# Kernel tuning notes

Hardware: AMD Instinct MI355X
Metric: run time of the kernel (lower is better)

The kernel has to match this reference:

```python
import jax, jax.numpy as jnp
import numpy as np

B, T, D = 2, 2048, 1024
D_LABEL = D // 2
N_LABELS = 50


def setup_inputs() -> dict:
    key = jax.random.key(0)
    ks = jax.random.split(key, 10)
    dep = jax.random.normal(ks[0], (B, T, D), dtype=jnp.float32)
    head = jax.random.normal(ks[1], (B, T + 1, D), dtype=jnp.float32)
    head_indices = jax.random.randint(ks[2], (B, T), 0, T + 1)
    mask = jnp.ones((B, T), dtype=bool)
    # learned params
    lim_p = 1.0 / np.sqrt(D)
    dep_W = jax.random.uniform(ks[3], (D_LABEL, D), minval=-lim_p, maxval=lim_p, dtype=jnp.float32)
    dep_b = jax.random.uniform(ks[4], (D_LABEL,), minval=-lim_p, maxval=lim_p, dtype=jnp.float32)
    head_W = jax.random.uniform(ks[5], (D_LABEL, D), minval=-lim_p, maxval=lim_p, dtype=jnp.float32)
    head_b = jax.random.uniform(ks[6], (D_LABEL,), minval=-lim_p, maxval=lim_p, dtype=jnp.float32)
    # xavier_uniform over last two dims of W
    lim_w = np.sqrt(6.0 / (D_LABEL + D_LABEL))
    W = jax.random.uniform(ks[7], (N_LABELS, D_LABEL, D_LABEL), minval=-lim_w, maxval=lim_w, dtype=jnp.float32)
    bias = jnp.zeros((N_LABELS,), dtype=jnp.float32)
    return {"dep": dep, "head": head, "head_indices": head_indices, "mask": mask,
            "dep_W": dep_W, "dep_b": dep_b, "head_W": head_W, "head_b": head_b,
            "W": W, "bias": bias}


def reference(dep, head, head_indices, mask, dep_W, dep_b, head_W, head_b, W, bias):
    # project to label space [B,T,d_label] / [B,T+1,d_label]
    dep_label = jnp.einsum('btd,ed->bte', dep, dep_W) + dep_b
    head_label = jnp.einsum('btd,ed->bte', head, head_W) + head_b
    # gather predicted head rep per token: [B,T,d_label]
    selected = jnp.take_along_axis(head_label, head_indices[..., None], axis=1)
    # biaffine scoring: dep^T W_n head for each label n -> [B,T,n_labels]
    logits = jnp.einsum('btd,nde,bte->btn', dep_label, W, selected)
    return logits + bias[None, None, :]
```

## Files before the change

kernel.cpp:

```cpp
#include <hip/hip_runtime.h>
#include <hip/hip_bf16.h>
#include <cstdint>

typedef __bf16 bf16;
typedef bf16 bf16x8 __attribute__((ext_vector_type(8)));
typedef float f32x4 __attribute__((ext_vector_type(4)));

#define NTOK 4096
#define DLBL 512
#define NLAB 50

__device__ inline bf16x8 cvt8(float4 a, float4 b) {
  bf16x8 r;
  r[0] = (bf16)a.x; r[1] = (bf16)a.y; r[2] = (bf16)a.z; r[3] = (bf16)a.w;
  r[4] = (bf16)b.x; r[5] = (bf16)b.y; r[6] = (bf16)b.z; r[7] = (bf16)b.w;
  return r;
}

__device__ __forceinline__ void gl16(const bf16* g, void* l) {
  __builtin_amdgcn_global_load_lds(
      (const __attribute__((address_space(1))) void*)g,
      (__attribute__((address_space(3))) void*)l, 16, 0, 0);
}

__device__ void projA_body(int bidx, const float* __restrict__ Wp,
                           const float* __restrict__ X,
                           const float* __restrict__ bv,
                           bf16* __restrict__ outT, char* lds) {
  char* ldsA = lds;
  char* ldsB = lds + 10240;
  const int tid = threadIdx.x, l = tid & 63, w = tid >> 6;
  const int tokbase = (bidx >> 2) * 64;
  const int ebase   = (bidx & 3) * 128;
  const int wr = w & 1, wc = w >> 1;
  f32x4 acc[4][2] = {};
  const int arow = tid >> 1, ahalf = tid & 1;
  const int brow = tid >> 2, bgr = tid & 3;
  const float* aS = Wp + (size_t)(ebase + arow) * 1024 + ahalf * 16;
  const float* bS = X  + (size_t)(tokbase + brow) * 1024 + bgr * 8;
  const int lo = (l & 15) * 80 + (l >> 4) * 16;
  for (int kb = 0; kb < 1024; kb += 32) {
    float4 a0 = *(const float4*)(aS + kb);
    float4 a1 = *(const float4*)(aS + kb + 4);
    float4 a2 = *(const float4*)(aS + kb + 8);
    float4 a3 = *(const float4*)(aS + kb + 12);
    float4 b0 = *(const float4*)(bS + kb);
    float4 b1 = *(const float4*)(bS + kb + 4);
    *(bf16x8*)(ldsA + arow * 80 + ahalf * 32)      = cvt8(a0, a1);
    *(bf16x8*)(ldsA + arow * 80 + ahalf * 32 + 16) = cvt8(a2, a3);
    *(bf16x8*)(ldsB + brow * 80 + bgr * 16)        = cvt8(b0, b1);
    __syncthreads();
    bf16x8 aF[4], bF[2];
#pragma unroll
    for (int i = 0; i < 4; ++i) aF[i] = *(bf16x8*)(ldsA + (wr * 64 + i * 16) * 80 + lo);
#pragma unroll
    for (int j = 0; j < 2; ++j) bF[j] = *(bf16x8*)(ldsB + (wc * 32 + j * 16) * 80 + lo);
#pragma unroll
    for (int i = 0; i < 4; ++i)
#pragma unroll
      for (int j = 0; j < 2; ++j)
        acc[i][j] = __builtin_amdgcn_mfma_f32_16x16x32_bf16(aF[i], bF[j], acc[i][j], 0, 0, 0);
    __syncthreads();
  }
#pragma unroll
  for (int i = 0; i < 4; ++i)
#pragma unroll
    for (int j = 0; j < 2; ++j)
#pragma unroll
      for (int r = 0; r < 4; ++r) {
        int eg = ebase + wr * 64 + i * 16 + (l >> 4) * 4 + r;
        int tg = tokbase + wc * 32 + j * 16 + (l & 15);
        outT[(size_t)eg * NTOK + tg] = (bf16)(acc[i][j][r] + bv[eg]);
      }
}

__device__ void projB_body(int bidx, const float* __restrict__ head,
                           const int* __restrict__ hidx,
                           const float* __restrict__ Wp,
                           const float* __restrict__ bv,
                           bf16* __restrict__ selO, char* lds) {
  char* ldsA = lds;
  char* ldsB = lds + 10240;
  const int tid = threadIdx.x, l = tid & 63, w = tid >> 6;
  const int tokbase = (bidx >> 3) * 128;
  const int ebase   = (bidx & 7) * 64;
  const int wr = w & 1, wc = w >> 1;
  f32x4 acc[4][2] = {};
  const int arow = tid >> 1, ahalf = tid & 1;
  const int brow = tid >> 2, bgr = tid & 3;
  const int flat = tokbase + arow;
  const int bb = flat >> 11;
  const int hv = hidx[flat];
  const float* aS = head + ((size_t)bb * 2049 + hv) * 1024 + ahalf * 16;
  const float* bS = Wp + (size_t)(ebase + brow) * 1024 + bgr * 8;
  const int lo = (l & 15) * 80 + (l >> 4) * 16;
  for (int kb = 0; kb < 1024; kb += 32) {
    float4 a0 = *(const float4*)(aS + kb);
    float4 a1 = *(const float4*)(aS + kb + 4);
    float4 a2 = *(const float4*)(aS + kb + 8);
    float4 a3 = *(const float4*)(aS + kb + 12);
    float4 b0 = *(const float4*)(bS + kb);
    float4 b1 = *(const float4*)(bS + kb + 4);
    *(bf16x8*)(ldsA + arow * 80 + ahalf * 32)      = cvt8(a0, a1);
    *(bf16x8*)(ldsA + arow * 80 + ahalf * 32 + 16) = cvt8(a2, a3);
    *(bf16x8*)(ldsB + brow * 80 + bgr * 16)        = cvt8(b0, b1);
    __syncthreads();
    bf16x8 aF[4], bF[2];
#pragma unroll
    for (int i = 0; i < 4; ++i) aF[i] = *(bf16x8*)(ldsA + (wr * 64 + i * 16) * 80 + lo);
#pragma unroll
    for (int j = 0; j < 2; ++j) bF[j] = *(bf16x8*)(ldsB + (wc * 32 + j * 16) * 80 + lo);
#pragma unroll
    for (int i = 0; i < 4; ++i)
#pragma unroll
      for (int j = 0; j < 2; ++j)
        acc[i][j] = __builtin_amdgcn_mfma_f32_16x16x32_bf16(aF[i], bF[j], acc[i][j], 0, 0, 0);
    __syncthreads();
  }
#pragma unroll
  for (int i = 0; i < 4; ++i)
#pragma unroll
    for (int j = 0; j < 2; ++j)
#pragma unroll
      for (int r = 0; r < 4; ++r) {
        int tg = tokbase + wr * 64 + i * 16 + (l >> 4) * 4 + r;
        int eg = ebase + wc * 32 + j * 16 + (l & 15);
        selO[(size_t)tg * DLBL + eg] = (bf16)(acc[i][j][r] + bv[eg]);
      }
}

__global__ __launch_bounds__(256) void prep_k(const float* __restrict__ W,
                                              bf16* __restrict__ Wb,
                                              const float* __restrict__ dep_W,
                                              const float* __restrict__ dep,
                                              const float* __restrict__ dep_b,
                                              bf16* __restrict__ depT,
                                              const float* __restrict__ head,
                                              const int* __restrict__ hidx,
                                              const float* __restrict__ head_W,
                                              const float* __restrict__ head_b,
                                              bf16* __restrict__ selB) {
  __shared__ char lds[15360];
  const int b = blockIdx.x;
  if (b < 256) {
    projA_body(b, dep_W, dep, dep_b, depT, lds);
  } else if (b < 512) {
    projB_body(b - 256, head, hidx, head_W, head_b, selB, lds);
  } else {
    int i = (b - 512) * 256 + threadIdx.x;
    const float4* s = (const float4*)W + (size_t)i * 2;
    float4 a = s[0], c = s[1];
    *(bf16x8*)(Wb + (size_t)i * 8) = cvt8(a, c);
  }
}

__global__ __launch_bounds__(256, 2) void biaff_k(const bf16* __restrict__ Wb,
                                                  const bf16* __restrict__ sel,
                                                  const bf16* __restrict__ depT,
                                                  float* __restrict__ parts) {
  __shared__ char lds[73728];
  const int tid = threadIdx.x, l = tid & 63, w = tid >> 6;

  const int lin = blockIdx.x;
  const int xcd = lin & 7, idx = lin >> 3;
  const int sub = idx % 25;
  const int bx  = idx / 25;
  const int combo = xcd * 25 + sub;
  const int n  = combo % 50;
  const int dz = combo / 50;
  const int tokbase = bx * 256;
  const int dbase   = dz * 128;

  const int wd = w >> 1, wt = w & 1;
  f32x4 acc[4][8] = {};

  const int srow = l >> 2;
  const int schunk = ((l & 3) ^ ((l >> 3) & 3)) * 8;
  const bf16* aG = Wb  + ((size_t)(n * DLBL + dbase + w * 32 + srow)) * DLBL + schunk;
  const bf16* bG = sel + ((size_t)(tokbase + w * 64 + srow)) * DLBL + schunk;
  const int aOff = w * 2048;
  const int bOff = 8192 + w * 4096;

  const int lq = l & 15, lh = l >> 4;
  const int ro = lh ^ ((lq >> 1) & 3);
  const char* rdA = lds + (wd * 64 + lq) * 64 + ro * 16;
  const char* rdB = lds + 8192 + (wt * 128 + lq) * 64 + ro * 16;

#define STG(T) do { \
    const bf16* a_ = aG + (T) * 32; \
    const bf16* b_ = bG + (T) * 32; \
    char* la_ = lds + ((T) % 3) * 24576 + aOff; \
    char* lb_ = lds + ((T) % 3) * 24576 + bOff; \
    gl16(a_, la_);            gl16(a_ + 16 * DLBL, la_ + 1024); \
    gl16(b_, lb_);            gl16(b_ + 16 * DLBL, lb_ + 1024); \
    gl16(b_ + 32 * DLBL, lb_ + 2048); gl16(b_ + 48 * DLBL, lb_ + 3072); \
  } while (0)
#define WAITV(N) asm volatile("s_waitcnt vmcnt(" #N ")" ::: "memory")
#define PHASE(T, DOSTG, DOWV6, DOWV0, DOBAR) do { \
    const char* cA = rdA + ((T) % 3) * 24576; \
    const char* cB = rdB + ((T) % 3) * 24576; \
    bf16x8 aF[4], bF[8]; \
    _Pragma("unroll") \
    for (int i = 0; i < 4; ++i) aF[i] = *(const bf16x8*)(cA + i * 1024); \
    _Pragma("unroll") \
    for (int j = 0; j < 8; ++j) bF[j] = *(const bf16x8*)(cB + j * 1024); \
    if (DOSTG) STG((T) + 2); \
    __builtin_amdgcn_s_setprio(1); \
    _Pragma("unroll") \
    for (int i = 0; i < 4; ++i) \
      _Pragma("unroll") \
      for (int j = 0; j < 8; ++j) \
        acc[i][j] = __builtin_amdgcn_mfma_f32_16x16x32_bf16(aF[i], bF[j], acc[i][j], 0, 0, 0); \
    __builtin_amdgcn_s_setprio(0); \
    if (DOWV6) WAITV(6); \
    if (DOWV0) WAITV(0); \
    if (DOBAR) __builtin_amdgcn_s_barrier(); \
  } while (0)

  STG(0); STG(1);
  WAITV(6);
  __builtin_amdgcn_s_barrier();

  PHASE(0, 1, 1, 0, 1);  PHASE(1, 1, 1, 0, 1);  PHASE(2, 1, 1, 0, 1);
  PHASE(3, 1, 1, 0, 1);  PHASE(4, 1, 1, 0, 1);  PHASE(5, 1, 1, 0, 1);
  PHASE(6, 1, 1, 0, 1);  PHASE(7, 1, 1, 0, 1);  PHASE(8, 1, 1, 0, 1);
  PHASE(9, 1, 1, 0, 1);  PHASE(10, 1, 1, 0, 1); PHASE(11, 1, 1, 0, 1);
  PHASE(12, 1, 1, 0, 1); PHASE(13, 1, 1, 0, 1);
  PHASE(14, 0, 0, 1, 1);
  PHASE(15, 0, 0, 0, 0);

#undef PHASE
#undef WAITV
#undef STG

  float p[8] = {0.f, 0.f, 0.f, 0.f, 0.f, 0.f, 0.f, 0.f};
#pragma unroll
  for (int j = 0; j < 8; ++j) {
    const int tg = tokbase + wt * 128 + j * 16 + lq;
#pragma unroll
    for (int i = 0; i < 4; ++i)
#pragma unroll
      for (int r = 0; r < 4; ++r) {
        int dg = dbase + wd * 64 + i * 16 + lh * 4 + r;
        p[j] += acc[i][j][r] * (float)depT[(size_t)dg * NTOK + tg];
      }
  }
#pragma unroll
  for (int j = 0; j < 8; ++j) {
    p[j] += __shfl_xor(p[j], 16);
    p[j] += __shfl_xor(p[j], 32);
  }
  if (l < 16) {
#pragma unroll
    for (int j = 0; j < 8; ++j) {
      int tg = tokbase + wt * 128 + j * 16 + l;
      parts[(size_t)(dz * 2 + wd) * 204800 + (size_t)tg * NLAB + n] = p[j];
    }
  }
}

__global__ __launch_bounds__(256) void fin_k(const float* __restrict__ parts,
                                             const float* __restrict__ bias,
                                             float* __restrict__ out) {
  int i = blockIdx.x * 256 + threadIdx.x;
  float v = 0.f;
#pragma unroll
  for (int q = 0; q < 8; ++q) v += parts[(size_t)q * 204800 + i];
  out[i] = v + bias[i % NLAB];
}

extern "C" void kernel_launch(void* const* d_in, const int* in_sizes, int n_in,
                              void* d_out, int out_size, void* d_ws, size_t ws_size,
                              hipStream_t stream) {
  const float* dep    = (const float*)d_in[0];
  const float* head   = (const float*)d_in[1];
  const int*   hidx   = (const int*)d_in[2];
  const float* dep_W  = (const float*)d_in[4];
  const float* dep_b  = (const float*)d_in[5];
  const float* head_W = (const float*)d_in[6];
  const float* head_b = (const float*)d_in[7];
  const float* W      = (const float*)d_in[8];
  const float* bias   = (const float*)d_in[9];
  float* out = (float*)d_out;

  char* ws = (char*)d_ws;
  bf16*  Wb    = (bf16*)(ws);
  bf16*  depT  = (bf16*)(ws + 26214400);
  bf16*  selB  = (bf16*)(ws + 30408704);
  float* parts = (float*)(ws + 34603008);
  if (ws_size < (size_t)41156608) return;

  hipLaunchKernelGGL(prep_k, dim3(6912), dim3(256), 0, stream,
                     W, Wb, dep_W, dep, dep_b, depT, head, hidx, head_W, head_b, selB);
  hipLaunchKernelGGL(biaff_k, dim3(3200), dim3(256), 0, stream, Wb, selB, depT, parts);
  hipLaunchKernelGGL(fin_k, dim3(800), dim3(256), 0, stream, parts, bias, out);
}
```

Baseline: 163.3 us.

## Enlarge biaffine GEMM tile to 256x256 with 512-thread blocks and double buffering

The biaffine kernel now uses 512-thread blocks that each compute a 256(d) x 256(token) tile, replacing the 128x256 tile, with K steps of 64 split into two half-steps and a 2-stage LDS double buffer instead of a 3-stage ring. The grid is halved and the XCD-to-block mapping is reworked so paired XCDs share label slices across token blocks. Fewer d-splits mean fewer partial sums to write and to reduce in fin_k. In exchange, each block holds 128 KB of LDS and more barriers per K step, which could lower occupancy and expose more load latency.

New measurement: 177.3 us. +8.6%, slower.

```diff
diff --git a/kernel.cpp b/kernel.cpp
--- a/kernel.cpp
+++ b/kernel.cpp
@@ -154,107 +154,126 @@
   }
 }
 
-__global__ __launch_bounds__(256, 2) void biaff_k(const bf16* __restrict__ Wb,
+__global__ __launch_bounds__(512, 2) void biaff_k(const bf16* __restrict__ Wb,
                                                   const bf16* __restrict__ sel,
                                                   const bf16* __restrict__ depT,
                                                   float* __restrict__ parts) {
-  __shared__ char lds[73728];
+  __shared__ char lds[131072];
   const int tid = threadIdx.x, l = tid & 63, w = tid >> 6;
 
   const int lin = blockIdx.x;
-  const int xcd = lin & 7, idx = lin >> 3;
-  const int sub = idx % 25;
-  const int bx  = idx / 25;
-  const int combo = xcd * 25 + sub;
+  const int xcd = lin & 7, j5 = lin >> 3;
+  const int g = xcd >> 1, h = xcd & 1;
+  const int combo = g * 25 + (j5 % 25);
+  const int bx = (j5 / 25) * 2 + h;
   const int n  = combo % 50;
   const int dz = combo / 50;
   const int tokbase = bx * 256;
-  const int dbase   = dz * 128;
-
-  const int wd = w >> 1, wt = w & 1;
-  f32x4 acc[4][8] = {};
+
+  const int wd = w >> 2, wt = w & 3;
+  f32x4 acc[8][4] = {};
 
   const int srow = l >> 2;
   const int schunk = ((l & 3) ^ ((l >> 3) & 3)) * 8;
-  const bf16* aG = Wb  + ((size_t)(n * DLBL + dbase + w * 32 + srow)) * DLBL + schunk;
-  const bf16* bG = sel + ((size_t)(tokbase + w * 64 + srow)) * DLBL + schunk;
+  const bf16* aG = Wb  + ((size_t)(n * DLBL + dz * 256 + w * 32 + srow)) * DLBL + schunk;
+  const bf16* bG = sel + ((size_t)(tokbase + w * 32 + srow)) * DLBL + schunk;
   const int aOff = w * 2048;
-  const int bOff = 8192 + w * 4096;
 
   const int lq = l & 15, lh = l >> 4;
   const int ro = lh ^ ((lq >> 1) & 3);
-  const char* rdA = lds + (wd * 64 + lq) * 64 + ro * 16;
-  const char* rdB = lds + 8192 + (wt * 128 + lq) * 64 + ro * 16;
-
-#define STG(T) do { \
-    const bf16* a_ = aG + (T) * 32; \
-    const bf16* b_ = bG + (T) * 32; \
-    char* la_ = lds + ((T) % 3) * 24576 + aOff; \
-    char* lb_ = lds + ((T) % 3) * 24576 + bOff; \
-    gl16(a_, la_);            gl16(a_ + 16 * DLBL, la_ + 1024); \
-    gl16(b_, lb_);            gl16(b_ + 16 * DLBL, lb_ + 1024); \
-    gl16(b_ + 32 * DLBL, lb_ + 2048); gl16(b_ + 48 * DLBL, lb_ + 3072); \
+  const char* rdA = lds + (wd * 128 + lq) * 64 + ro * 16;
+  const char* rdB = lds + 16384 + (wt * 64 + lq) * 64 + ro * 16;
+
+#define STG_A(T, KK) do { \
+    const bf16* s_ = aG + (T) * 64 + (KK) * 32; \
+    char* d_ = lds + (((T) & 1) * 65536) + (KK) * 32768 + aOff; \
+    gl16(s_, d_); gl16(s_ + 16 * DLBL, d_ + 1024); \
+  } while (0)
+#define STG_B(T, KK) do { \
+    const bf16* s_ = bG + (T) * 64 + (KK) * 32; \
+    char* d_ = lds + (((T) & 1) * 65536) + 16384 + (KK) * 32768 + aOff; \
+    gl16(s_, d_); gl16(s_ + 16 * DLBL, d_ + 1024); \
   } while (0)
 #define WAITV(N) asm volatile("s_waitcnt vmcnt(" #N ")" ::: "memory")
-#define PHASE(T, DOSTG, DOWV6, DOWV0, DOBAR) do { \
-    const char* cA = rdA + ((T) % 3) * 24576; \
-    const char* cB = rdB + ((T) % 3) * 24576; \
-    bf16x8 aF[4], bF[8]; \
-    _Pragma("unroll") \
-    for (int i = 0; i < 4; ++i) aF[i] = *(const bf16x8*)(cA + i * 1024); \
-    _Pragma("unroll") \
-    for (int j = 0; j < 8; ++j) bF[j] = *(const bf16x8*)(cB + j * 1024); \
-    if (DOSTG) STG((T) + 2); \
+#define RDA(KK, M) do { _Pragma("unroll") for (int i = 0; i < 4; ++i) \
+    aF[i] = *(const bf16x8*)(rdA + cb + (KK) * 32768 + (M) * 4096 + i * 1024); } while (0)
+#define RDB(KK) do { _Pragma("unroll") for (int jj = 0; jj < 4; ++jj) \
+    bF[jj] = *(const bf16x8*)(rdB + cb + (KK) * 32768 + jj * 1024); } while (0)
+#define MM(M) do { \
     __builtin_amdgcn_s_setprio(1); \
-    _Pragma("unroll") \
-    for (int i = 0; i < 4; ++i) \
-      _Pragma("unroll") \
-      for (int j = 0; j < 8; ++j) \
-        acc[i][j] = __builtin_amdgcn_mfma_f32_16x16x32_bf16(aF[i], bF[j], acc[i][j], 0, 0, 0); \
+    _Pragma("unroll") for (int i = 0; i < 4; ++i) \
+      _Pragma("unroll") for (int jj = 0; jj < 4; ++jj) \
+        acc[(M) * 4 + i][jj] = __builtin_amdgcn_mfma_f32_16x16x32_bf16(aF[i], bF[jj], acc[(M) * 4 + i][jj], 0, 0, 0); \
     __builtin_amdgcn_s_setprio(0); \
-    if (DOWV6) WAITV(6); \
-    if (DOWV0) WAITV(0); \
-    if (DOBAR) __builtin_amdgcn_s_barrier(); \
   } while (0)
-
-  STG(0); STG(1);
-  WAITV(6);
-  __builtin_amdgcn_s_barrier();
-
-  PHASE(0, 1, 1, 0, 1);  PHASE(1, 1, 1, 0, 1);  PHASE(2, 1, 1, 0, 1);
-  PHASE(3, 1, 1, 0, 1);  PHASE(4, 1, 1, 0, 1);  PHASE(5, 1, 1, 0, 1);
-  PHASE(6, 1, 1, 0, 1);  PHASE(7, 1, 1, 0, 1);  PHASE(8, 1, 1, 0, 1);
-  PHASE(9, 1, 1, 0, 1);  PHASE(10, 1, 1, 0, 1); PHASE(11, 1, 1, 0, 1);
-  PHASE(12, 1, 1, 0, 1); PHASE(13, 1, 1, 0, 1);
-  PHASE(14, 0, 0, 1, 1);
-  PHASE(15, 0, 0, 0, 0);
-
-#undef PHASE
+#define BAR __builtin_amdgcn_s_barrier()
+
+#define TILE(T, DOSTG, V1, DOV3) do { \
+    const int cb = ((T) & 1) * 65536; \
+    bf16x8 aF[4], bF[4]; \
+     \
+    RDA(0, 0); RDB(0); \
+    if (DOSTG) STG_A((T) + 1, 0); \
+    BAR; MM(0); BAR; \
+     \
+    RDA(0, 1); \
+    if (DOSTG) STG_B((T) + 1, 0); \
+    BAR; MM(1); WAITV(V1); BAR; \
+     \
+    RDA(1, 0); RDB(1); \
+    if (DOSTG) STG_A((T) + 1, 1); \
+    BAR; MM(0); BAR; \
+     \
+    RDA(1, 1); \
+    if (DOSTG) STG_B((T) + 1, 1); \
+    BAR; MM(1); \
+    if (DOV3) { WAITV(4); } \
+    if (DOV3) { BAR; } \
+  } while (0)
+
+  STG_A(0, 0); STG_B(0, 0); STG_A(0, 1); STG_B(0, 1);
+  WAITV(0);
+  BAR;
+
+  TILE(0, 1, 4, 1);
+  TILE(1, 1, 4, 1);
+  TILE(2, 1, 4, 1);
+  TILE(3, 1, 4, 1);
+  TILE(4, 1, 4, 1);
+  TILE(5, 1, 4, 1);
+  TILE(6, 1, 4, 1);
+  TILE(7, 0, 0, 0);
+
+#undef TILE
+#undef BAR
+#undef MM
+#undef RDB
+#undef RDA
 #undef WAITV
-#undef STG
-
-  float p[8] = {0.f, 0.f, 0.f, 0.f, 0.f, 0.f, 0.f, 0.f};
-#pragma unroll
-  for (int j = 0; j < 8; ++j) {
-    const int tg = tokbase + wt * 128 + j * 16 + lq;
-#pragma unroll
-    for (int i = 0; i < 4; ++i)
-#pragma unroll
-      for (int r = 0; r < 4; ++r) {
-        int dg = dbase + wd * 64 + i * 16 + lh * 4 + r;
-        p[j] += acc[i][j][r] * (float)depT[(size_t)dg * NTOK + tg];
-      }
-  }
-#pragma unroll
-  for (int j = 0; j < 8; ++j) {
-    p[j] += __shfl_xor(p[j], 16);
-    p[j] += __shfl_xor(p[j], 32);
+#undef STG_B
+#undef STG_A
+
+  const bf16* dT = depT + (size_t)(dz * 256 + wd * 128) * NTOK;
+  float p[4] = {0.f, 0.f, 0.f, 0.f};
+#pragma unroll
+  for (int jj = 0; jj < 4; ++jj) {
+    const int tg = tokbase + wt * 64 + jj * 16 + lq;
+#pragma unroll
+    for (int i = 0; i < 8; ++i)
+#pragma unroll
+      for (int r = 0; r < 4; ++r)
+        p[jj] += acc[i][jj][r] * (float)dT[(size_t)(i * 16 + lh * 4 + r) * NTOK + tg];
+  }
+#pragma unroll
+  for (int jj = 0; jj < 4; ++jj) {
+    p[jj] += __shfl_xor(p[jj], 16);
+    p[jj] += __shfl_xor(p[jj], 32);
   }
   if (l < 16) {
 #pragma unroll
-    for (int j = 0; j < 8; ++j) {
-      int tg = tokbase + wt * 128 + j * 16 + l;
-      parts[(size_t)(dz * 2 + wd) * 204800 + (size_t)tg * NLAB + n] = p[j];
+    for (int jj = 0; jj < 4; ++jj) {
+      int tg = tokbase + wt * 64 + jj * 16 + l;
+      parts[(size_t)(dz * 2 + wd) * 204800 + (size_t)tg * NLAB + n] = p[jj];
     }
   }
 }
@@ -265,7 +284,7 @@
   int i = blockIdx.x * 256 + threadIdx.x;
   float v = 0.f;
 #pragma unroll
-  for (int q = 0; q < 8; ++q) v += parts[(size_t)q * 204800 + i];
+  for (int q = 0; q < 4; ++q) v += parts[(size_t)q * 204800 + i];
   out[i] = v + bias[i % NLAB];
 }
 
@@ -288,10 +307,10 @@
   bf16*  depT  = (bf16*)(ws + 26214400);
   bf16*  selB  = (bf16*)(ws + 30408704);
   float* parts = (float*)(ws + 34603008);
-  if (ws_size < (size_t)41156608) return;
+  if (ws_size < (size_t)37879808) return;
 
   hipLaunchKernelGGL(prep_k, dim3(6912), dim3(256), 0, stream,
                      W, Wb, dep_W, dep, dep_b, depT, head, hidx, head_W, head_b, selB);
-  hipLaunchKernelGGL(biaff_k, dim3(3200), dim3(256), 0, stream, Wb, selB, depT, parts);
+  hipLaunchKernelGGL(biaff_k, dim3(1600), dim3(512), 0, stream, Wb, selB, depT, parts);
   hipLaunchKernelGGL(fin_k, dim3(800), dim3(256), 0, stream, parts, bias, out);
 }
```

## Switch biaffine kernel to 32x32 MFMA with 8 waves and in-block reduction

Applied to the files above, without the earlier changes.

The biaffine kernel now runs 8 waves per block, each computing a 64x64 sub-tile with 32x32x16 bf16 MFMAs instead of a 128x128-per-4-waves tile with 16x16x32 MFMAs. The two d-halves are reduced through LDS inside the block, so the partial-sum buffer and the final reduction shrink from 8 to 4 slices. The dep projection now writes token-major output so the epilogue can read contiguous bf16x4 vectors, and the two projection bodies are merged into one. The aim is fewer LDS fragment reads per MFMA, lower per-wave register pressure, and less partial-sum traffic. The cost is extra barriers and an LDS round trip in the epilogue, and register use with 512 threads at 2 blocks per CU may be tight.

After: 193.4 us. +18.5%, slower.

```diff
diff --git a/kernel.cpp b/kernel.cpp
--- a/kernel.cpp
+++ b/kernel.cpp
@@ -3,8 +3,10 @@
 #include <cstdint>
 
 typedef __bf16 bf16;
+typedef bf16 bf16x4 __attribute__((ext_vector_type(4)));
 typedef bf16 bf16x8 __attribute__((ext_vector_type(8)));
 typedef float f32x4 __attribute__((ext_vector_type(4)));
+typedef float f32x16 __attribute__((ext_vector_type(16)));
 
 #define NTOK 4096
 #define DLBL 512
@@ -23,62 +25,11 @@
       (__attribute__((address_space(3))) void*)l, 16, 0, 0);
 }
 
-__device__ void projA_body(int bidx, const float* __restrict__ Wp,
-                           const float* __restrict__ X,
-                           const float* __restrict__ bv,
-                           bf16* __restrict__ outT, char* lds) {
-  char* ldsA = lds;
-  char* ldsB = lds + 10240;
-  const int tid = threadIdx.x, l = tid & 63, w = tid >> 6;
-  const int tokbase = (bidx >> 2) * 64;
-  const int ebase   = (bidx & 3) * 128;
-  const int wr = w & 1, wc = w >> 1;
-  f32x4 acc[4][2] = {};
-  const int arow = tid >> 1, ahalf = tid & 1;
-  const int brow = tid >> 2, bgr = tid & 3;
-  const float* aS = Wp + (size_t)(ebase + arow) * 1024 + ahalf * 16;
-  const float* bS = X  + (size_t)(tokbase + brow) * 1024 + bgr * 8;
-  const int lo = (l & 15) * 80 + (l >> 4) * 16;
-  for (int kb = 0; kb < 1024; kb += 32) {
-    float4 a0 = *(const float4*)(aS + kb);
-    float4 a1 = *(const float4*)(aS + kb + 4);
-    float4 a2 = *(const float4*)(aS + kb + 8);
-    float4 a3 = *(const float4*)(aS + kb + 12);
-    float4 b0 = *(const float4*)(bS + kb);
-    float4 b1 = *(const float4*)(bS + kb + 4);
-    *(bf16x8*)(ldsA + arow * 80 + ahalf * 32)      = cvt8(a0, a1);
-    *(bf16x8*)(ldsA + arow * 80 + ahalf * 32 + 16) = cvt8(a2, a3);
-    *(bf16x8*)(ldsB + brow * 80 + bgr * 16)        = cvt8(b0, b1);
-    __syncthreads();
-    bf16x8 aF[4], bF[2];
-#pragma unroll
-    for (int i = 0; i < 4; ++i) aF[i] = *(bf16x8*)(ldsA + (wr * 64 + i * 16) * 80 + lo);
-#pragma unroll
-    for (int j = 0; j < 2; ++j) bF[j] = *(bf16x8*)(ldsB + (wc * 32 + j * 16) * 80 + lo);
-#pragma unroll
-    for (int i = 0; i < 4; ++i)
-#pragma unroll
-      for (int j = 0; j < 2; ++j)
-        acc[i][j] = __builtin_amdgcn_mfma_f32_16x16x32_bf16(aF[i], bF[j], acc[i][j], 0, 0, 0);
-    __syncthreads();
-  }
-#pragma unroll
-  for (int i = 0; i < 4; ++i)
-#pragma unroll
-    for (int j = 0; j < 2; ++j)
-#pragma unroll
-      for (int r = 0; r < 4; ++r) {
-        int eg = ebase + wr * 64 + i * 16 + (l >> 4) * 4 + r;
-        int tg = tokbase + wc * 32 + j * 16 + (l & 15);
-        outT[(size_t)eg * NTOK + tg] = (bf16)(acc[i][j][r] + bv[eg]);
-      }
-}
-
-__device__ void projB_body(int bidx, const float* __restrict__ head,
-                           const int* __restrict__ hidx,
-                           const float* __restrict__ Wp,
-                           const float* __restrict__ bv,
-                           bf16* __restrict__ selO, char* lds) {
+__device__ void proj_body(int bidx, const float* __restrict__ rows,
+                          const int* __restrict__ hidx, int rowstride,
+                          const float* __restrict__ Wp,
+                          const float* __restrict__ bv,
+                          bf16* __restrict__ outN, char* lds) {
   char* ldsA = lds;
   char* ldsB = lds + 10240;
   const int tid = threadIdx.x, l = tid & 63, w = tid >> 6;
@@ -90,8 +41,8 @@
   const int brow = tid >> 2, bgr = tid & 3;
   const int flat = tokbase + arow;
   const int bb = flat >> 11;
-  const int hv = hidx[flat];
-  const float* aS = head + ((size_t)bb * 2049 + hv) * 1024 + ahalf * 16;
+  const int rv = hidx ? hidx[flat] + bb * rowstride : flat;
+  const float* aS = rows + (size_t)rv * 1024 + ahalf * 16;
   const float* bS = Wp + (size_t)(ebase + brow) * 1024 + bgr * 8;
   const int lo = (l & 15) * 80 + (l >> 4) * 16;
   for (int kb = 0; kb < 1024; kb += 32) {
@@ -125,7 +76,7 @@
       for (int r = 0; r < 4; ++r) {
         int tg = tokbase + wr * 64 + i * 16 + (l >> 4) * 4 + r;
         int eg = ebase + wc * 32 + j * 16 + (l & 15);
-        selO[(size_t)tg * DLBL + eg] = (bf16)(acc[i][j][r] + bv[eg]);
+        outN[(size_t)tg * DLBL + eg] = (bf16)(acc[i][j][r] + bv[eg]);
       }
 }
 
@@ -134,7 +85,7 @@
                                               const float* __restrict__ dep_W,
                                               const float* __restrict__ dep,
                                               const float* __restrict__ dep_b,
-                                              bf16* __restrict__ depT,
+                                              bf16* __restrict__ depN,
                                               const float* __restrict__ head,
                                               const int* __restrict__ hidx,
                                               const float* __restrict__ head_W,
@@ -143,9 +94,9 @@
   __shared__ char lds[15360];
   const int b = blockIdx.x;
   if (b < 256) {
-    projA_body(b, dep_W, dep, dep_b, depT, lds);
+    proj_body(b, dep, nullptr, 0, dep_W, dep_b, depN, lds);
   } else if (b < 512) {
-    projB_body(b - 256, head, hidx, head_W, head_b, selB, lds);
+    proj_body(b - 256, head, hidx, 2049, head_W, head_b, selB, lds);
   } else {
     int i = (b - 512) * 256 + threadIdx.x;
     const float4* s = (const float4*)W + (size_t)i * 2;
@@ -154,9 +105,9 @@
   }
 }
 
-__global__ __launch_bounds__(256, 2) void biaff_k(const bf16* __restrict__ Wb,
+__global__ __launch_bounds__(512, 2) void biaff_k(const bf16* __restrict__ Wb,
                                                   const bf16* __restrict__ sel,
-                                                  const bf16* __restrict__ depT,
+                                                  const bf16* __restrict__ depN,
                                                   float* __restrict__ parts) {
   __shared__ char lds[73728];
   const int tid = threadIdx.x, l = tid & 63, w = tid >> 6;
@@ -171,54 +122,59 @@
   const int tokbase = bx * 256;
   const int dbase   = dz * 128;
 
-  const int wd = w >> 1, wt = w & 1;
-  f32x4 acc[4][8] = {};
+  const int wd = w >> 2, wt = w & 3;
+  f32x16 acc[2][2] = {};
 
   const int srow = l >> 2;
   const int schunk = ((l & 3) ^ ((l >> 3) & 3)) * 8;
-  const bf16* aG = Wb  + ((size_t)(n * DLBL + dbase + w * 32 + srow)) * DLBL + schunk;
-  const bf16* bG = sel + ((size_t)(tokbase + w * 64 + srow)) * DLBL + schunk;
-  const int aOff = w * 2048;
-  const int bOff = 8192 + w * 4096;
-
-  const int lq = l & 15, lh = l >> 4;
-  const int ro = lh ^ ((lq >> 1) & 3);
-  const char* rdA = lds + (wd * 64 + lq) * 64 + ro * 16;
-  const char* rdB = lds + 8192 + (wt * 128 + lq) * 64 + ro * 16;
+  const bf16* aG = Wb  + ((size_t)(n * DLBL + dbase + w * 16 + srow)) * DLBL + schunk;
+  const bf16* bG = sel + ((size_t)(tokbase + w * 32 + srow)) * DLBL + schunk;
+  const int aOff = w * 1024;
+  const int bOff = 8192 + w * 2048;
+
+  const int r31 = l & 31, l5 = l >> 5;
+  const int xr = (r31 >> 1) & 3;
+  const int cAoff = (wd * 64 + r31) * 64 + ((l5 ^ xr) * 16);
+  const int cBoff = 8192 + (wt * 64 + r31) * 64 + ((l5 ^ xr) * 16);
 
 #define STG(T) do { \
     const bf16* a_ = aG + (T) * 32; \
     const bf16* b_ = bG + (T) * 32; \
     char* la_ = lds + ((T) % 3) * 24576 + aOff; \
     char* lb_ = lds + ((T) % 3) * 24576 + bOff; \
-    gl16(a_, la_);            gl16(a_ + 16 * DLBL, la_ + 1024); \
-    gl16(b_, lb_);            gl16(b_ + 16 * DLBL, lb_ + 1024); \
-    gl16(b_ + 32 * DLBL, lb_ + 2048); gl16(b_ + 48 * DLBL, lb_ + 3072); \
+    gl16(a_, la_); \
+    gl16(b_, lb_); \
+    gl16(b_ + 16 * DLBL, lb_ + 1024); \
   } while (0)
 #define WAITV(N) asm volatile("s_waitcnt vmcnt(" #N ")" ::: "memory")
-#define PHASE(T, DOSTG, DOWV6, DOWV0, DOBAR) do { \
-    const char* cA = rdA + ((T) % 3) * 24576; \
-    const char* cB = rdB + ((T) % 3) * 24576; \
-    bf16x8 aF[4], bF[8]; \
-    _Pragma("unroll") \
-    for (int i = 0; i < 4; ++i) aF[i] = *(const bf16x8*)(cA + i * 1024); \
-    _Pragma("unroll") \
-    for (int j = 0; j < 8; ++j) bF[j] = *(const bf16x8*)(cB + j * 1024); \
+#define PHASE(T, DOSTG, DOWV3, DOWV0, DOBAR) do { \
+    const char* base_ = lds + ((T) % 3) * 24576; \
+    bf16x8 a00 = *(const bf16x8*)(base_ + cAoff); \
+    bf16x8 a01 = *(const bf16x8*)(base_ + (cAoff ^ 32)); \
+    bf16x8 a10 = *(const bf16x8*)(base_ + (cAoff + 2048)); \
+    bf16x8 a11 = *(const bf16x8*)(base_ + ((cAoff + 2048) ^ 32)); \
+    bf16x8 b00 = *(const bf16x8*)(base_ + cBoff); \
+    bf16x8 b01 = *(const bf16x8*)(base_ + (cBoff ^ 32)); \
+    bf16x8 b10 = *(const bf16x8*)(base_ + (cBoff + 2048)); \
+    bf16x8 b11 = *(const bf16x8*)(base_ + ((cBoff + 2048) ^ 32)); \
     if (DOSTG) STG((T) + 2); \
     __builtin_amdgcn_s_setprio(1); \
-    _Pragma("unroll") \
-    for (int i = 0; i < 4; ++i) \
-      _Pragma("unroll") \
-      for (int j = 0; j < 8; ++j) \
-        acc[i][j] = __builtin_amdgcn_mfma_f32_16x16x32_bf16(aF[i], bF[j], acc[i][j], 0, 0, 0); \
+    acc[0][0] = __builtin_amdgcn_mfma_f32_32x32x16_bf16(a00, b00, acc[0][0], 0, 0, 0); \
+    acc[0][1] = __builtin_amdgcn_mfma_f32_32x32x16_bf16(a00, b10, acc[0][1], 0, 0, 0); \
+    acc[1][0] = __builtin_amdgcn_mfma_f32_32x32x16_bf16(a10, b00, acc[1][0], 0, 0, 0); \
+    acc[1][1] = __builtin_amdgcn_mfma_f32_32x32x16_bf16(a10, b10, acc[1][1], 0, 0, 0); \
+    acc[0][0] = __builtin_amdgcn_mfma_f32_32x32x16_bf16(a01, b01, acc[0][0], 0, 0, 0); \
+    acc[0][1] = __builtin_amdgcn_mfma_f32_32x32x16_bf16(a01, b11, acc[0][1], 0, 0, 0); \
+    acc[1][0] = __builtin_amdgcn_mfma_f32_32x32x16_bf16(a11, b01, acc[1][0], 0, 0, 0); \
+    acc[1][1] = __builtin_amdgcn_mfma_f32_32x32x16_bf16(a11, b11, acc[1][1], 0, 0, 0); \
     __builtin_amdgcn_s_setprio(0); \
-    if (DOWV6) WAITV(6); \
+    if (DOWV3) WAITV(3); \
     if (DOWV0) WAITV(0); \
     if (DOBAR) __builtin_amdgcn_s_barrier(); \
   } while (0)
 
   STG(0); STG(1);
-  WAITV(6);
+  WAITV(3);
   __builtin_amdgcn_s_barrier();
 
   PHASE(0, 1, 1, 0, 1);  PHASE(1, 1, 1, 0, 1);  PHASE(2, 1, 1, 0, 1);
@@ -233,29 +189,38 @@
 #undef WAITV
 #undef STG
 
-  float p[8] = {0.f, 0.f, 0.f, 0.f, 0.f, 0.f, 0.f, 0.f};
-#pragma unroll
-  for (int j = 0; j < 8; ++j) {
-    const int tg = tokbase + wt * 128 + j * 16 + lq;
-#pragma unroll
-    for (int i = 0; i < 4; ++i)
-#pragma unroll
-      for (int r = 0; r < 4; ++r) {
-        int dg = dbase + wd * 64 + i * 16 + lh * 4 + r;
-        p[j] += acc[i][j][r] * (float)depT[(size_t)dg * NTOK + tg];
+  float p0 = 0.f, p1 = 0.f;
+  const bf16* dN0 = depN + (size_t)(tokbase + wt * 64 + r31) * DLBL
+                    + dbase + wd * 64 + l5 * 4;
+  const bf16* dN1 = dN0 + (size_t)32 * DLBL;
+#pragma unroll
+  for (int ti = 0; ti < 2; ++ti)
+#pragma unroll
+    for (int q = 0; q < 4; ++q) {
+      bf16x4 v0 = *(const bf16x4*)(dN0 + ti * 32 + q * 8);
+      bf16x4 v1 = *(const bf16x4*)(dN1 + ti * 32 + q * 8);
+#pragma unroll
+      for (int m = 0; m < 4; ++m) {
+        p0 += acc[ti][0][q * 4 + m] * (float)v0[m];
+        p1 += acc[ti][1][q * 4 + m] * (float)v1[m];
       }
-  }
-#pragma unroll
-  for (int j = 0; j < 8; ++j) {
-    p[j] += __shfl_xor(p[j], 16);
-    p[j] += __shfl_xor(p[j], 32);
-  }
-  if (l < 16) {
-#pragma unroll
-    for (int j = 0; j < 8; ++j) {
-      int tg = tokbase + wt * 128 + j * 16 + l;
-      parts[(size_t)(dz * 2 + wd) * 204800 + (size_t)tg * NLAB + n] = p[j];
     }
+  p0 += __shfl_xor(p0, 32);
+  p1 += __shfl_xor(p1, 32);
+
+  __syncthreads();
+  float* lf = (float*)lds;
+  if (wd == 1 && l < 32) {
+    lf[(w - 4) * 64 + l]      = p0;
+    lf[(w - 4) * 64 + 32 + l] = p1;
+  }
+  __syncthreads();
+  if (wd == 0 && l < 32) {
+    p0 += lf[w * 64 + l];
+    p1 += lf[w * 64 + 32 + l];
+    const size_t tg0 = tokbase + wt * 64 + r31;
+    parts[(size_t)dz * 204800 + tg0 * NLAB + n]        = p0;
+    parts[(size_t)dz * 204800 + (tg0 + 32) * NLAB + n] = p1;
   }
 }
 
@@ -265,7 +230,7 @@
   int i = blockIdx.x * 256 + threadIdx.x;
   float v = 0.f;
 #pragma unroll
-  for (int q = 0; q < 8; ++q) v += parts[(size_t)q * 204800 + i];
+  for (int q = 0; q < 4; ++q) v += parts[(size_t)q * 204800 + i];
   out[i] = v + bias[i % NLAB];
 }
 
@@ -285,13 +250,13 @@
 
   char* ws = (char*)d_ws;
   bf16*  Wb    = (bf16*)(ws);
-  bf16*  depT  = (bf16*)(ws + 26214400);
+  bf16*  depN  = (bf16*)(ws + 26214400);
   bf16*  selB  = (bf16*)(ws + 30408704);
   float* parts = (float*)(ws + 34603008);
-  if (ws_size < (size_t)41156608) return;
+  if (ws_size < (size_t)37879808) return;
 
   hipLaunchKernelGGL(prep_k, dim3(6912), dim3(256), 0, stream,
-                     W, Wb, dep_W, dep, dep_b, depT, head, hidx, head_W, head_b, selB);
-  hipLaunchKernelGGL(biaff_k, dim3(3200), dim3(256), 0, stream, Wb, selB, depT, parts);
+                     W, Wb, dep_W, dep, dep_b, depN, head, hidx, head_W, head_b, selB);
+  hipLaunchKernelGGL(biaff_k, dim3(3200), dim3(512), 0, stream, Wb, selB, depN, parts);
   hipLaunchKernelGGL(fin_k, dim3(800), dim3(256), 0, stream, parts, bias, out);
 }
```
